# Kernel optimization log

Hardware: AMD Instinct MI355X
Metric: run time of the kernel (lower is better)

## Reference

```python
import jax, jax.numpy as jnp
import numpy as np

HIDDEN = 2048
NUM_ROUTED = 24          # num_routed_experts(6) * segmentation_factor(4)
ROUTED_INTER = 512       # intermediate_dim(2048) // segmentation_factor(4)
NUM_SHARED = 2
SHARED_INTER = 2048
TOP_K = 6


def setup_inputs() -> dict:
    key = jax.random.key(0)
    ks = jax.random.split(key, 8)
    std = 0.02
    x = jax.random.normal(ks[0], (2, 2048, HIDDEN), dtype=jnp.float32)
    gate_w = jax.random.normal(ks[1], (NUM_ROUTED, HIDDEN), dtype=jnp.float32) * (0.02 / np.sqrt(HIDDEN))
    shared_w1 = jax.random.normal(ks[2], (NUM_SHARED, HIDDEN, SHARED_INTER), dtype=jnp.float32) * std
    shared_w3 = jax.random.normal(ks[3], (NUM_SHARED, HIDDEN, SHARED_INTER), dtype=jnp.float32) * std
    shared_w2 = jax.random.normal(ks[4], (NUM_SHARED, SHARED_INTER, HIDDEN), dtype=jnp.float32) * std
    routed_w1 = jax.random.normal(ks[5], (NUM_ROUTED, HIDDEN, ROUTED_INTER), dtype=jnp.float32) * std
    routed_w3 = jax.random.normal(ks[6], (NUM_ROUTED, HIDDEN, ROUTED_INTER), dtype=jnp.float32) * std
    routed_w2 = jax.random.normal(ks[7], (NUM_ROUTED, ROUTED_INTER, HIDDEN), dtype=jnp.float32) * std
    return {"x": x, "gate_w": gate_w,
            "shared_w1": shared_w1, "shared_w2": shared_w2, "shared_w3": shared_w3,
            "routed_w1": routed_w1, "routed_w2": routed_w2, "routed_w3": routed_w3}


def _swiglu_ffn(x, w1, w2, w3):
    # x: [..., n, h]; w1,w3: [..., h, i]; w2: [..., i, h]  (dropout inactive at eval)
    h = jax.nn.silu(jnp.einsum('nh,ehi->eni', x, w1)) * jnp.einsum('nh,ehi->eni', x, w3)
    return jnp.einsum('eni,eih->enh', h, w2)


def reference(x, gate_w, shared_w1, shared_w2, shared_w3, routed_w1, routed_w2, routed_w3):
    B, S, H = x.shape
    x_flat = x.reshape(-1, H)                       # [N, H]
    N = x_flat.shape[0]

    # shared experts (summed)
    shared_out = _swiglu_ffn(x_flat, shared_w1, shared_w2, shared_w3).sum(axis=0)  # [N, H]

    # routing (eval mode: no bias added to logits, aux_loss = 0)
    scores = jax.nn.sigmoid(x_flat @ gate_w.T)      # [N, E]
    top_scores, top_idx = jax.lax.top_k(scores, TOP_K)
    top_weights = top_scores / (top_scores.sum(-1, keepdims=True) + 1e-9)  # [N, K]

    # dense dispatch/combine weights [N, E] (indices unique per row)
    dense_w = jnp.zeros((N, NUM_ROUTED), dtype=x.dtype)
    dense_w = dense_w.at[jnp.arange(N)[:, None], top_idx].set(top_weights)

    # run every routed expert on all tokens, combine with routing weights
    expert_out = _swiglu_ffn(x_flat, routed_w1, routed_w2, routed_w3)  # [E, N, H]
    combined = jnp.einsum('ne,enh->nh', dense_w, expert_out)

    output = (shared_out + combined).reshape(B, S, H)
    aux_loss = jnp.float32(0.0)  # eval mode
    return output, aux_loss
```

## Files before the change

### kernel.cpp

```cpp
#include <hip/hip_runtime.h>
#include <hip/hip_bf16.h>

#define HID   2048
#define NTOK  4096
#define NEXP  24
#define SHCOL 4096
#define TOPK  6
#define NSLOT (NTOK * TOPK)

typedef __bf16 bf16_t;
typedef __bf16 bf16x8 __attribute__((ext_vector_type(8)));
typedef __bf16 bf16x4 __attribute__((ext_vector_type(4)));
typedef float  f32x4  __attribute__((ext_vector_type(4)));

__device__ __forceinline__ void async_copy16(const bf16_t* g, bf16_t* l) {
  __builtin_amdgcn_global_load_lds(
      (const __attribute__((address_space(1))) unsigned int*)g,
      (__attribute__((address_space(3))) unsigned int*)l,
      16, 0, 0);
}
template<int N> __device__ __forceinline__ void wait_vm() {
  asm volatile("s_waitcnt vmcnt(%0)" :: "n"(N) : "memory");
}
__device__ __forceinline__ void memfence_sched() { asm volatile("" ::: "memory"); }
__device__ __forceinline__ void bar() {
  memfence_sched();
  __builtin_amdgcn_s_barrier();
  memfence_sched();
}

__device__ __forceinline__ bf16x8 frag32(const bf16_t* region, int row, int cc) {
  return *(const bf16x8*)(region + row * 32 + ((cc ^ ((row >> 1) & 3)) << 3));
}

__global__ void cast_x_kernel(const float* __restrict__ x, bf16_t* __restrict__ xb) {
  int i = blockIdx.x * 256 + threadIdx.x;
  float4 v = ((const float4*)x)[i];
  bf16x4 o = { (bf16_t)v.x, (bf16_t)v.y, (bf16_t)v.z, (bf16_t)v.w };
  ((bf16x4*)xb)[i] = o;
}

__global__ __launch_bounds__(256) void transpose_cast_v2(
    const float* __restrict__ src, bf16_t* __restrict__ dst,
    int C, long dstStride, long srcExpStride, long dstExpStride) {
  __shared__ float t[64][68];
  const int e = blockIdx.z;
  src += (long)e * srcExpStride;
  dst += (long)e * dstExpStride;
  const int c0 = blockIdx.x * 64, r0 = blockIdx.y * 64;
  const int tid = threadIdx.x;
  {
    const int tr = tid >> 4, tc = tid & 15;
#pragma unroll
    for (int p = 0; p < 4; ++p) {
      const int r = p * 16 + tr;
      const float4 v = *(const float4*)(src + (long)(r0 + r) * C + c0 + tc * 4);
      *(float4*)&t[r][tc * 4] = v;
    }
  }
  __syncthreads();
  {
    const int l8 = tid & 7, rb = l8 * 8;
#pragma unroll
    for (int p = 0; p < 2; ++p) {
      const int c = p * 32 + (tid >> 3);
      bf16x8 o;
#pragma unroll
      for (int s = 0; s < 8; ++s) o[s] = (bf16_t)t[rb + s][c];
      *(bf16x8*)(dst + (long)(c0 + c) * dstStride + r0 + rb) = o;
    }
  }
}

__global__ void gate_topk(const float* __restrict__ x, const float* __restrict__ gw,
                          int* __restrict__ tk_idx, float* __restrict__ tk_w,
                          float* __restrict__ aux) {
  int lane = threadIdx.x & 63;
  int wave = threadIdx.x >> 6;
  int token = blockIdx.x * 4 + wave;
  const float* xr = x + (long)token * HID;
  float xv[32];
#pragma unroll
  for (int i = 0; i < 32; ++i) xv[i] = xr[lane + i * 64];
  float sc[NEXP];
#pragma unroll
  for (int e = 0; e < NEXP; ++e) {
    const float* g = gw + (long)e * HID;
    float s = 0.f;
#pragma unroll
    for (int i = 0; i < 32; ++i) s += xv[i] * g[lane + i * 64];
#pragma unroll
    for (int off = 32; off > 0; off >>= 1) s += __shfl_down(s, off);
    sc[e] = s;
  }
  if (lane == 0) {
    float sg[NEXP];
#pragma unroll
    for (int e = 0; e < NEXP; ++e) sg[e] = 1.0f / (1.0f + expf(-sc[e]));
    unsigned taken = 0;
    int   sel[TOPK];
    float sw[TOPK];
    float sum = 0.f;
    for (int k = 0; k < TOPK; ++k) {
      float best = -1.f; int bi = 0;
#pragma unroll
      for (int e = 0; e < NEXP; ++e) {
        bool avail = !(taken & (1u << e));
        if (avail && sg[e] > best) { best = sg[e]; bi = e; }
      }
      taken |= (1u << bi);
      sel[k] = bi; sw[k] = best; sum += best;
    }
    float inv = 1.0f / (sum + 1e-9f);
#pragma unroll
    for (int k = 0; k < TOPK; ++k) {
      tk_idx[token * TOPK + k] = sel[k];
      tk_w[token * TOPK + k]   = sw[k] * inv;
    }
  }
  if (blockIdx.x == 0 && threadIdx.x == 0) *aux = 0.0f;
}

__global__ void dispatch(const int* __restrict__ tk_idx, const float* __restrict__ tk_w,
                         int* __restrict__ perm, float* __restrict__ wslot,
                         int* __restrict__ slot_of, int* __restrict__ meta,
                         int* __restrict__ uptab, int* __restrict__ dntab) {
  __shared__ int cnt[NEXP], cnt2[NEXP], off[NEXP + 1];
  int tid = threadIdx.x;
  if (tid < NEXP) { cnt[tid] = 0; cnt2[tid] = 0; }
  __syncthreads();
  for (int i = tid; i < NSLOT; i += 1024) atomicAdd(&cnt[tk_idx[i]], 1);
  __syncthreads();
  if (tid == 0) {
    int o = 0, un = 0, dn = 0;
    for (int e = 0; e < NEXP; ++e) {
      off[e] = o;
      int c = cnt[e];
      for (int r0 = 0; r0 < c; r0 += 256) uptab[un++] = (e << 16) | r0;
      for (int r0 = 0; r0 < c; r0 += 128) dntab[dn++] = (e << 16) | r0;
      o += c;
    }
    off[NEXP] = o;
    meta[0] = un; meta[1] = dn;
    for (int e = 0; e < NEXP; ++e) { meta[8 + e] = cnt[e]; meta[32 + e] = off[e]; }
  }
  __syncthreads();
  for (int i = tid; i < NSLOT; i += 1024) {
    int e = tk_idx[i];
    int loc = atomicAdd(&cnt2[e], 1);
    int slot = off[e] + loc;
    perm[slot] = i / TOPK;
    wslot[slot] = tk_w[i];
    slot_of[i] = slot;
  }
}

__global__ __launch_bounds__(512, 2) void gemm_up(
    const bf16_t* __restrict__ xb, const bf16_t* __restrict__ w1t,
    const bf16_t* __restrict__ w3t, bf16_t* __restrict__ hsh,
    bf16_t* __restrict__ hr, const int* __restrict__ perm,
    const float* __restrict__ wslot, const int* __restrict__ meta,
    const int* __restrict__ uptab) {
  __shared__ bf16_t lds[4 * 16384];
  const int bid = blockIdx.x;
  const int tid  = threadIdx.x;
  const int lane = tid & 63;
  const int wave = tid >> 6;
  const int wm = wave >> 2;
  const int wc = wave & 3;
  const bool role_sh = bid < 512;
  int m0 = 0, j0 = 0, jc = 0, M = 256, bslot = 0;
  const bf16_t *b1G, *b3G;
  if (role_sh) {
    m0 = (bid >> 5) * 256; j0 = (bid & 31) * 128;
    b1G = w1t + (long)j0 * HID;
    b3G = w3t + (long)j0 * HID;
  } else {
    int t = bid - 512;
    int rt = t >> 2; jc = t & 3;
    if (rt >= meta[0]) return;
    int pk = uptab[rt];
    int e = pk >> 16, row0 = pk & 0xffff;
    bslot = meta[32 + e] + row0;
    M = min(256, meta[8 + e] - row0);
    int col = SHCOL + e * 512 + jc * 128;
    b1G = w1t + (long)col * HID;
    b3G = w3t + (long)col * HID;
  }
  const bf16_t* gsrc[4];
  int loff[4];
#pragma unroll
  for (int it = 0; it < 4; ++it) {
    int idx = it * 512 + tid;
    if (idx < 1024) {
      int r = idx >> 2, c = idx & 3;
      long rowbase;
      if (role_sh) rowbase = (long)(m0 + r) * HID;
      else         rowbase = (long)perm[bslot + ((r < M) ? r : 0)] * HID;
      gsrc[it] = xb + rowbase + ((c ^ ((r >> 1) & 3)) << 3);
      loff[it] = idx << 3;
    } else if (idx < 1536) {
      int i2 = idx - 1024; int r = i2 >> 2, c = i2 & 3;
      gsrc[it] = b1G + (long)r * HID + ((c ^ ((r >> 1) & 3)) << 3);
      loff[it] = 8192 + (i2 << 3);
    } else {
      int i2 = idx - 1536; int r = i2 >> 2, c = i2 & 3;
      gsrc[it] = b3G + (long)r * HID + ((c ^ ((r >> 1) & 3)) << 3);
      loff[it] = 12288 + (i2 << 3);
    }
  }
  auto STAGE = [&](int t) {
    bf16_t* sb = lds + (t & 3) * 16384;
#pragma unroll
    for (int it = 0; it < 4; ++it)
      async_copy16(gsrc[it] + t * 32, sb + loff[it]);
  };

  f32x4 acc1[8][2] = {};
  f32x4 acc3[8][2] = {};
  const int NT = HID / 32;
  STAGE(0); STAGE(1);
  wait_vm<4>();
  __syncthreads();
  const int rA = wm * 128 + (lane & 15);
  const int rB = wc * 32 + (lane & 15);
  const int cc = lane >> 4;
  for (int t = 0; t < NT; ++t) {
    const bf16_t* sb = lds + (t & 3) * 16384;
    bf16x8 a[4], b1[2], b3[2];
#pragma unroll
    for (int fm = 0; fm < 4; ++fm) a[fm] = frag32(sb, rA + fm * 16, cc);
#pragma unroll
    for (int fn = 0; fn < 2; ++fn) {
      b1[fn] = frag32(sb + 8192,  rB + fn * 16, cc);
      b3[fn] = frag32(sb + 12288, rB + fn * 16, cc);
    }
    if (t + 2 < NT) STAGE(t + 2);
    bar();
    __builtin_amdgcn_s_setprio(1);
#pragma unroll
    for (int fn = 0; fn < 2; ++fn)
#pragma unroll
      for (int fm = 0; fm < 4; ++fm) {
        acc1[fm][fn] = __builtin_amdgcn_mfma_f32_16x16x32_bf16(a[fm], b1[fn], acc1[fm][fn], 0, 0, 0);
        acc3[fm][fn] = __builtin_amdgcn_mfma_f32_16x16x32_bf16(a[fm], b3[fn], acc3[fm][fn], 0, 0, 0);
      }
    __builtin_amdgcn_s_setprio(0);
    bar();
    bf16x8 a2[4];
#pragma unroll
    for (int fm = 0; fm < 4; ++fm) a2[fm] = frag32(sb, rA + 64 + fm * 16, cc);
    bar();
    __builtin_amdgcn_s_setprio(1);
#pragma unroll
    for (int fn = 0; fn < 2; ++fn)
#pragma unroll
      for (int fm = 0; fm < 4; ++fm) {
        acc1[4 + fm][fn] = __builtin_amdgcn_mfma_f32_16x16x32_bf16(a2[fm], b1[fn], acc1[4 + fm][fn], 0, 0, 0);
        acc3[4 + fm][fn] = __builtin_amdgcn_mfma_f32_16x16x32_bf16(a2[fm], b3[fn], acc3[4 + fm][fn], 0, 0, 0);
      }
    __builtin_amdgcn_s_setprio(0);
    memfence_sched();
    if (t < NT - 2) wait_vm<4>();
    else            wait_vm<0>();
    bar();
  }
  const int mloc_base = wm * 128 + ((lane >> 4) << 2);
  const int cloc = wc * 32 + (lane & 15);
#pragma unroll
  for (int fm = 0; fm < 8; ++fm) {
#pragma unroll
    for (int jj = 0; jj < 4; ++jj) {
      const int mloc = mloc_base + fm * 16 + jj;
      if (role_sh) {
        bf16_t* dst = hsh + (long)(m0 + mloc) * SHCOL + j0 + cloc;
#pragma unroll
        for (int fn = 0; fn < 2; ++fn) {
          const float u1 = acc1[fm][fn][jj];
          const float u3 = acc3[fm][fn][jj];
          dst[fn * 16] = (bf16_t)((u1 / (1.0f + __expf(-u1))) * u3);
        }
      } else if (mloc < M) {
        const int slot = bslot + mloc;
        const float w = wslot[slot];
        bf16_t* dst = hr + (long)slot * 512 + jc * 128 + cloc;
#pragma unroll
        for (int fn = 0; fn < 2; ++fn) {
          const float u1 = acc1[fm][fn][jj];
          const float u3 = acc3[fm][fn][jj];
          dst[fn * 16] = (bf16_t)((u1 / (1.0f + __expf(-u1))) * u3 * w);
        }
      }
    }
  }
}

__global__ __launch_bounds__(512, 2) void gemm_down(
    const bf16_t* __restrict__ hsh, const bf16_t* __restrict__ w2ts,
    const bf16_t* __restrict__ hr, const bf16_t* __restrict__ rw2t,
    float* __restrict__ sout, bf16_t* __restrict__ y,
    const int* __restrict__ meta, const int* __restrict__ dntab) {
  __shared__ bf16_t lds[4 * 12288];
  const int bid = blockIdx.x;
  const int tid  = threadIdx.x;
  const int lane = tid & 63;
  const int wave = tid >> 6;
  const int wm = wave >> 2;
  const int wc = wave & 3;
  const bool role_sh = bid < 256;
  int m0 = 0, n0, M = 128, bslot = 0, NT;
  const bf16_t *aG, *bG;
  long lda, ldb;
  if (role_sh) {
    m0 = (bid >> 3) * 128; n0 = (bid & 7) * 256;
    aG = hsh + (long)m0 * SHCOL; lda = SHCOL;
    bG = w2ts + (long)n0 * SHCOL; ldb = SHCOL;
    NT = SHCOL / 32;
  } else {
    int t = bid - 256;
    int rt = t >> 3; n0 = (t & 7) * 256;
    if (rt >= meta[1]) return;
    int pk = dntab[rt];
    int e = pk >> 16, row0 = pk & 0xffff;
    bslot = meta[32 + e] + row0;
    M = min(128, meta[8 + e] - row0);
    aG = hr + (long)bslot * 512; lda = 512;
    bG = rw2t + (long)e * (2048L * 512) + (long)n0 * 512; ldb = 512;
    NT = 512 / 32;
  }
  const bf16_t* gsrc[3];
  int loff[3];
#pragma unroll
  for (int it = 0; it < 3; ++it) {
    int idx = it * 512 + tid;
    if (idx < 512) {
      int r = idx >> 2, c = idx & 3;
      gsrc[it] = aG + (long)r * lda + ((c ^ ((r >> 1) & 3)) << 3);
      loff[it] = idx << 3;
    } else {
      int i2 = idx - 512; int r = i2 >> 2, c = i2 & 3;
      gsrc[it] = bG + (long)r * ldb + ((c ^ ((r >> 1) & 3)) << 3);
      loff[it] = 4096 + (i2 << 3);
    }
  }
  auto STAGE = [&](int t) {
    bf16_t* sb = lds + (t & 3) * 12288;
#pragma unroll
    for (int it = 0; it < 3; ++it)
      async_copy16(gsrc[it] + t * 32, sb + loff[it]);
  };

  f32x4 acc[4][4] = {};
  STAGE(0); STAGE(1);
  wait_vm<3>();
  __syncthreads();
  const int rA = wm * 64 + (lane & 15);
  const int rB = wc * 64 + (lane & 15);
  const int cc = lane >> 4;
  for (int t = 0; t < NT; ++t) {
    const bf16_t* sb = lds + (t & 3) * 12288;
    bf16x8 a[4], b[4];
#pragma unroll
    for (int fm = 0; fm < 4; ++fm) a[fm] = frag32(sb, rA + fm * 16, cc);
    b[0] = frag32(sb + 4096, rB, cc);
    b[1] = frag32(sb + 4096, rB + 16, cc);
    if (t + 2 < NT) STAGE(t + 2);
    bar();
    __builtin_amdgcn_s_setprio(1);
#pragma unroll
    for (int fn = 0; fn < 2; ++fn)
#pragma unroll
      for (int fm = 0; fm < 4; ++fm)
        acc[fm][fn] = __builtin_amdgcn_mfma_f32_16x16x32_bf16(a[fm], b[fn], acc[fm][fn], 0, 0, 0);
    __builtin_amdgcn_s_setprio(0);
    bar();
    b[2] = frag32(sb + 4096, rB + 32, cc);
    b[3] = frag32(sb + 4096, rB + 48, cc);
    bar();
    __builtin_amdgcn_s_setprio(1);
#pragma unroll
    for (int fn = 2; fn < 4; ++fn)
#pragma unroll
      for (int fm = 0; fm < 4; ++fm)
        acc[fm][fn] = __builtin_amdgcn_mfma_f32_16x16x32_bf16(a[fm], b[fn], acc[fm][fn], 0, 0, 0);
    __builtin_amdgcn_s_setprio(0);
    memfence_sched();
    if (t < NT - 2) wait_vm<3>();
    else            wait_vm<0>();
    bar();
  }
  const int mloc_base = wm * 64 + ((lane >> 4) << 2);
  const int cbase = n0 + wc * 64 + (lane & 15);
#pragma unroll
  for (int fm = 0; fm < 4; ++fm)
#pragma unroll
    for (int jj = 0; jj < 4; ++jj) {
      const int mloc = mloc_base + fm * 16 + jj;
      if (role_sh) {
#pragma unroll
        for (int fn = 0; fn < 4; ++fn)
          sout[(long)(m0 + mloc) * HID + cbase + fn * 16] = acc[fm][fn][jj];
      } else if (mloc < M) {
#pragma unroll
        for (int fn = 0; fn < 4; ++fn)
          y[(long)(bslot + mloc) * HID + cbase + fn * 16] = (bf16_t)acc[fm][fn][jj];
      }
    }
}

__global__ void combine(const float* __restrict__ sout, const bf16_t* __restrict__ y,
                        const int* __restrict__ slot_of, float* __restrict__ out) {
  const int n = blockIdx.x;
  const int c0 = threadIdx.x * 8;
  float acc[8];
  const float4* sp = (const float4*)(sout + (long)n * HID + c0);
  float4 s0 = sp[0], s1 = sp[1];
  acc[0]=s0.x; acc[1]=s0.y; acc[2]=s0.z; acc[3]=s0.w;
  acc[4]=s1.x; acc[5]=s1.y; acc[6]=s1.z; acc[7]=s1.w;
#pragma unroll
  for (int k = 0; k < TOPK; ++k) {
    int slot = slot_of[n * TOPK + k];
    bf16x8 v = *(const bf16x8*)(y + (long)slot * HID + c0);
#pragma unroll
    for (int i = 0; i < 8; ++i) acc[i] += (float)v[i];
  }
  float4* op = (float4*)(out + (long)n * HID + c0);
  op[0] = make_float4(acc[0], acc[1], acc[2], acc[3]);
  op[1] = make_float4(acc[4], acc[5], acc[6], acc[7]);
}

__global__ void fill_sentinel(float* out, int n) {
  for (int i = blockIdx.x * 256 + threadIdx.x; i < n; i += gridDim.x * 256)
    out[i] = 12345.0f;
}

extern "C" void kernel_launch(void* const* d_in, const int* in_sizes, int n_in,
                              void* d_out, int out_size, void* d_ws, size_t ws_size,
                              hipStream_t stream) {
  (void)in_sizes; (void)n_in;
  const float* x   = (const float*)d_in[0];
  const float* gw  = (const float*)d_in[1];
  const float* sw1 = (const float*)d_in[2];
  const float* sw2 = (const float*)d_in[3];
  const float* sw3 = (const float*)d_in[4];
  const float* rw1 = (const float*)d_in[5];
  const float* rw2 = (const float*)d_in[6];
  const float* rw3 = (const float*)d_in[7];
  float* out = (float*)d_out;

  const size_t OFF_XB    = 0;
  const size_t OFF_W1T   = 16777216;
  const size_t OFF_W3T   = 83886080;
  const size_t OFF_W2TS  = 150994944;
  const size_t OFF_RW2T  = 167772160;
  const size_t OFF_HSH   = 218103808;
  const size_t OFF_HR    = 251658240;
  const size_t OFF_SOUT  = 277086208;
  const size_t OFF_TKI   = 310640640;
  const size_t OFF_TKW   = 310738944;
  const size_t OFF_PERM  = 310837248;
  const size_t OFF_WSLOT = 310935552;
  const size_t OFF_SLOTOF= 311033856;
  const size_t OFF_META  = 311132160;
  const size_t OFF_UPTAB = 311136256;
  const size_t OFF_DNTAB = 311140352;
  const size_t NEED      = 311148544;
  if (ws_size < NEED) {
    fill_sentinel<<<4096, 256, 0, stream>>>(out, out_size);
    return;
  }
  char* ws = (char*)d_ws;
  bf16_t* xb     = (bf16_t*)(ws + OFF_XB);
  bf16_t* w1t    = (bf16_t*)(ws + OFF_W1T);
  bf16_t* w3t    = (bf16_t*)(ws + OFF_W3T);
  bf16_t* w2ts   = (bf16_t*)(ws + OFF_W2TS);
  bf16_t* rw2t   = (bf16_t*)(ws + OFF_RW2T);
  bf16_t* hsh    = (bf16_t*)(ws + OFF_HSH);
  bf16_t* hr     = (bf16_t*)(ws + OFF_HR);
  float*  sout   = (float*)(ws + OFF_SOUT);
  bf16_t* y      = (bf16_t*)(ws + OFF_W1T);
  int*    tki    = (int*)(ws + OFF_TKI);
  float*  tkw    = (float*)(ws + OFF_TKW);
  int*    perm   = (int*)(ws + OFF_PERM);
  float*  wslot  = (float*)(ws + OFF_WSLOT);
  int*    slotof = (int*)(ws + OFF_SLOTOF);
  int*    meta   = (int*)(ws + OFF_META);
  int*    uptab  = (int*)(ws + OFF_UPTAB);
  int*    dntab  = (int*)(ws + OFF_DNTAB);

  cast_x_kernel<<<8192, 256, 0, stream>>>(x, xb);
  gate_topk<<<1024, 256, 0, stream>>>(x, gw, tki, tkw, out + (size_t)NTOK * HID);
  dispatch<<<1, 1024, 0, stream>>>(tki, tkw, perm, wslot, slotof, meta, uptab, dntab);

  transpose_cast_v2<<<dim3(32, 32, 2),  256, 0, stream>>>(sw1, w1t, 2048, 2048, 2048L*2048, 2048L*2048);
  transpose_cast_v2<<<dim3(8,  32, 24), 256, 0, stream>>>(rw1, w1t + (long)SHCOL*HID, 512, 2048, 2048L*512, 512L*2048);
  transpose_cast_v2<<<dim3(32, 32, 2),  256, 0, stream>>>(sw3, w3t, 2048, 2048, 2048L*2048, 2048L*2048);
  transpose_cast_v2<<<dim3(8,  32, 24), 256, 0, stream>>>(rw3, w3t + (long)SHCOL*HID, 512, 2048, 2048L*512, 512L*2048);
  transpose_cast_v2<<<dim3(32, 32, 2),  256, 0, stream>>>(sw2, w2ts, 2048, 4096, 2048L*2048, 2048);
  transpose_cast_v2<<<dim3(32, 8, 24),  256, 0, stream>>>(rw2, rw2t, 2048, 512, 512L*2048, 2048L*512);

  gemm_up<<<dim3(512 + 480), 512, 0, stream>>>(xb, w1t, w3t, hsh, hr, perm, wslot, meta, uptab);
  gemm_down<<<dim3(256 + 1728), 512, 0, stream>>>(hsh, w2ts, hr, rw2t, sout, y, meta, dntab);
  combine<<<dim3(NTOK), 256, 0, stream>>>(sout, y, slotof, out);
}
```

Measured before the change: 682.4 us.

## Merge cast/transpose kernels into one launch and cut per-iteration barriers in GEMMs

Folds the x cast and six weight transpose-cast launches into a single prep kernel indexed by flattened block id, removing launch gaps and tail effects between them. In gemm_up and gemm_down, the main loop is reorganised so each k-step waits on the async loads and barriers once at the top, with one mid-step barrier, replacing three barriers per iteration. gemm_down also drops from a 4-stage to a 3-stage LDS ring with stage issue after the barrier, which lowers LDS use. This adds risk around the vmcnt accounting and buffer reuse ordering with fewer barriers.

```diff
diff --git a/kernel.cpp b/kernel.cpp
--- a/kernel.cpp
+++ b/kernel.cpp
@@ -23,32 +23,15 @@
   asm volatile("s_waitcnt vmcnt(%0)" :: "n"(N) : "memory");
 }
 __device__ __forceinline__ void memfence_sched() { asm volatile("" ::: "memory"); }
-__device__ __forceinline__ void bar() {
-  memfence_sched();
-  __builtin_amdgcn_s_barrier();
-  memfence_sched();
-}
 
 __device__ __forceinline__ bf16x8 frag32(const bf16_t* region, int row, int cc) {
   return *(const bf16x8*)(region + row * 32 + ((cc ^ ((row >> 1) & 3)) << 3));
 }
 
-__global__ void cast_x_kernel(const float* __restrict__ x, bf16_t* __restrict__ xb) {
-  int i = blockIdx.x * 256 + threadIdx.x;
-  float4 v = ((const float4*)x)[i];
-  bf16x4 o = { (bf16_t)v.x, (bf16_t)v.y, (bf16_t)v.z, (bf16_t)v.w };
-  ((bf16x4*)xb)[i] = o;
-}
-
-__global__ __launch_bounds__(256) void transpose_cast_v2(
+__device__ __forceinline__ void tcast_tile(
     const float* __restrict__ src, bf16_t* __restrict__ dst,
-    int C, long dstStride, long srcExpStride, long dstExpStride) {
+    int C, long dstStride, int c0, int r0, int tid) {
   __shared__ float t[64][68];
-  const int e = blockIdx.z;
-  src += (long)e * srcExpStride;
-  dst += (long)e * dstExpStride;
-  const int c0 = blockIdx.x * 64, r0 = blockIdx.y * 64;
-  const int tid = threadIdx.x;
   {
     const int tr = tid >> 4, tc = tid & 15;
 #pragma unroll
@@ -70,6 +53,37 @@
       *(bf16x8*)(dst + (long)(c0 + c) * dstStride + r0 + rb) = o;
     }
   }
+}
+
+__global__ __launch_bounds__(256) void prep(
+    const float* __restrict__ x, bf16_t* __restrict__ xb,
+    const float* __restrict__ sw1, const float* __restrict__ rw1,
+    const float* __restrict__ sw3, const float* __restrict__ rw3,
+    const float* __restrict__ sw2, const float* __restrict__ rw2,
+    bf16_t* __restrict__ w1t, bf16_t* __restrict__ w3t,
+    bf16_t* __restrict__ w2ts, bf16_t* __restrict__ rw2t) {
+  int bid = blockIdx.x;
+  if (bid < 8192) {
+    int i = bid * 256 + threadIdx.x;
+    float4 v = ((const float4*)x)[i];
+    bf16x4 o = { (bf16_t)v.x, (bf16_t)v.y, (bf16_t)v.z, (bf16_t)v.w };
+    ((bf16x4*)xb)[i] = o;
+    return;
+  }
+  bid -= 8192;
+  const float* src; bf16_t* dst; int C; long dstStride, seS, deS; int BX, nPer;
+  if (bid < 2048)       { src=sw1; dst=w1t;                  C=2048; dstStride=2048; seS=2048L*2048; deS=2048L*2048; BX=32; nPer=1024; }
+  else if (bid < 8192)  { bid-=2048;  src=rw1; dst=w1t+(long)SHCOL*HID; C=512;  dstStride=2048; seS=2048L*512;  deS=512L*2048;  BX=8;  nPer=256; }
+  else if (bid < 10240) { bid-=8192;  src=sw3; dst=w3t;                 C=2048; dstStride=2048; seS=2048L*2048; deS=2048L*2048; BX=32; nPer=1024; }
+  else if (bid < 16384) { bid-=10240; src=rw3; dst=w3t+(long)SHCOL*HID; C=512;  dstStride=2048; seS=2048L*512;  deS=512L*2048;  BX=8;  nPer=256; }
+  else if (bid < 18432) { bid-=16384; src=sw2; dst=w2ts;                C=2048; dstStride=4096; seS=2048L*2048; deS=2048;       BX=32; nPer=1024; }
+  else                  { bid-=18432; src=rw2; dst=rw2t;                C=2048; dstStride=512;  seS=512L*2048;  deS=2048L*512;  BX=32; nPer=256; }
+  const int e  = bid / nPer;
+  const int rem = bid - e * nPer;
+  const int by = rem / BX;
+  const int bx = rem - by * BX;
+  tcast_tile(src + (long)e * seS, dst + (long)e * deS, C, dstStride,
+             bx * 64, by * 64, threadIdx.x);
 }
 
 __global__ void gate_topk(const float* __restrict__ x, const float* __restrict__ gw,
@@ -219,13 +233,17 @@
   f32x4 acc1[8][2] = {};
   f32x4 acc3[8][2] = {};
   const int NT = HID / 32;
-  STAGE(0); STAGE(1);
-  wait_vm<4>();
-  __syncthreads();
   const int rA = wm * 128 + (lane & 15);
   const int rB = wc * 32 + (lane & 15);
   const int cc = lane >> 4;
+  STAGE(0); STAGE(1);
   for (int t = 0; t < NT; ++t) {
+    if (t + 2 < NT) STAGE(t + 2);
+    if (t < NT - 2)       wait_vm<8>();
+    else if (t == NT - 2) wait_vm<4>();
+    else                  wait_vm<0>();
+    __builtin_amdgcn_s_barrier();
+    memfence_sched();
     const bf16_t* sb = lds + (t & 3) * 16384;
     bf16x8 a[4], b1[2], b3[2];
 #pragma unroll
@@ -235,8 +253,6 @@
       b1[fn] = frag32(sb + 8192,  rB + fn * 16, cc);
       b3[fn] = frag32(sb + 12288, rB + fn * 16, cc);
     }
-    if (t + 2 < NT) STAGE(t + 2);
-    bar();
     __builtin_amdgcn_s_setprio(1);
 #pragma unroll
     for (int fn = 0; fn < 2; ++fn)
@@ -246,11 +262,12 @@
         acc3[fm][fn] = __builtin_amdgcn_mfma_f32_16x16x32_bf16(a[fm], b3[fn], acc3[fm][fn], 0, 0, 0);
       }
     __builtin_amdgcn_s_setprio(0);
-    bar();
+    memfence_sched();
+    __builtin_amdgcn_s_barrier();
+    memfence_sched();
     bf16x8 a2[4];
 #pragma unroll
     for (int fm = 0; fm < 4; ++fm) a2[fm] = frag32(sb, rA + 64 + fm * 16, cc);
-    bar();
     __builtin_amdgcn_s_setprio(1);
 #pragma unroll
     for (int fn = 0; fn < 2; ++fn)
@@ -261,9 +278,6 @@
       }
     __builtin_amdgcn_s_setprio(0);
     memfence_sched();
-    if (t < NT - 2) wait_vm<4>();
-    else            wait_vm<0>();
-    bar();
   }
   const int mloc_base = wm * 128 + ((lane >> 4) << 2);
   const int cloc = wc * 32 + (lane & 15);
@@ -300,7 +314,7 @@
     const bf16_t* __restrict__ hr, const bf16_t* __restrict__ rw2t,
     float* __restrict__ sout, bf16_t* __restrict__ y,
     const int* __restrict__ meta, const int* __restrict__ dntab) {
-  __shared__ bf16_t lds[4 * 12288];
+  __shared__ bf16_t lds[3 * 12288];
   const int bid = blockIdx.x;
   const int tid  = threadIdx.x;
   const int lane = tid & 63;
@@ -344,28 +358,29 @@
     }
   }
   auto STAGE = [&](int t) {
-    bf16_t* sb = lds + (t & 3) * 12288;
+    bf16_t* sb = lds + (t % 3) * 12288;
 #pragma unroll
     for (int it = 0; it < 3; ++it)
       async_copy16(gsrc[it] + t * 32, sb + loff[it]);
   };
 
   f32x4 acc[4][4] = {};
-  STAGE(0); STAGE(1);
-  wait_vm<3>();
-  __syncthreads();
   const int rA = wm * 64 + (lane & 15);
   const int rB = wc * 64 + (lane & 15);
   const int cc = lane >> 4;
+  STAGE(0); STAGE(1);
   for (int t = 0; t < NT; ++t) {
-    const bf16_t* sb = lds + (t & 3) * 12288;
+    if (t + 1 < NT) wait_vm<3>();
+    else            wait_vm<0>();
+    __builtin_amdgcn_s_barrier();
+    memfence_sched();
+    if (t + 2 < NT) STAGE(t + 2);
+    const bf16_t* sb = lds + (t % 3) * 12288;
     bf16x8 a[4], b[4];
 #pragma unroll
     for (int fm = 0; fm < 4; ++fm) a[fm] = frag32(sb, rA + fm * 16, cc);
     b[0] = frag32(sb + 4096, rB, cc);
     b[1] = frag32(sb + 4096, rB + 16, cc);
-    if (t + 2 < NT) STAGE(t + 2);
-    bar();
     __builtin_amdgcn_s_setprio(1);
 #pragma unroll
     for (int fn = 0; fn < 2; ++fn)
@@ -373,10 +388,11 @@
       for (int fm = 0; fm < 4; ++fm)
         acc[fm][fn] = __builtin_amdgcn_mfma_f32_16x16x32_bf16(a[fm], b[fn], acc[fm][fn], 0, 0, 0);
     __builtin_amdgcn_s_setprio(0);
-    bar();
+    memfence_sched();
+    __builtin_amdgcn_s_barrier();
+    memfence_sched();
     b[2] = frag32(sb + 4096, rB + 32, cc);
     b[3] = frag32(sb + 4096, rB + 48, cc);
-    bar();
     __builtin_amdgcn_s_setprio(1);
 #pragma unroll
     for (int fn = 2; fn < 4; ++fn)
@@ -385,9 +401,6 @@
         acc[fm][fn] = __builtin_amdgcn_mfma_f32_16x16x32_bf16(a[fm], b[fn], acc[fm][fn], 0, 0, 0);
     __builtin_amdgcn_s_setprio(0);
     memfence_sched();
-    if (t < NT - 2) wait_vm<3>();
-    else            wait_vm<0>();
-    bar();
   }
   const int mloc_base = wm * 64 + ((lane >> 4) << 2);
   const int cbase = n0 + wc * 64 + (lane & 15);
@@ -488,16 +501,10 @@
   int*    uptab  = (int*)(ws + OFF_UPTAB);
   int*    dntab  = (int*)(ws + OFF_DNTAB);
 
-  cast_x_kernel<<<8192, 256, 0, stream>>>(x, xb);
   gate_topk<<<1024, 256, 0, stream>>>(x, gw, tki, tkw, out + (size_t)NTOK * HID);
   dispatch<<<1, 1024, 0, stream>>>(tki, tkw, perm, wslot, slotof, meta, uptab, dntab);
-
-  transpose_cast_v2<<<dim3(32, 32, 2),  256, 0, stream>>>(sw1, w1t, 2048, 2048, 2048L*2048, 2048L*2048);
-  transpose_cast_v2<<<dim3(8,  32, 24), 256, 0, stream>>>(rw1, w1t + (long)SHCOL*HID, 512, 2048, 2048L*512, 512L*2048);
-  transpose_cast_v2<<<dim3(32, 32, 2),  256, 0, stream>>>(sw3, w3t, 2048, 2048, 2048L*2048, 2048L*2048);
-  transpose_cast_v2<<<dim3(8,  32, 24), 256, 0, stream>>>(rw3, w3t + (long)SHCOL*HID, 512, 2048, 2048L*512, 512L*2048);
-  transpose_cast_v2<<<dim3(32, 32, 2),  256, 0, stream>>>(sw2, w2ts, 2048, 4096, 2048L*2048, 2048);
-  transpose_cast_v2<<<dim3(32, 8, 24),  256, 0, stream>>>(rw2, rw2t, 2048, 512, 512L*2048, 2048L*512);
+  prep<<<32768, 256, 0, stream>>>(x, xb, sw1, rw1, sw3, rw3, sw2, rw2,
+                                  w1t, w3t, w2ts, rw2t);
 
   gemm_up<<<dim3(512 + 480), 512, 0, stream>>>(xb, w1t, w3t, hsh, hr, perm, wslot, meta, uptab);
   gemm_down<<<dim3(256 + 1728), 512, 0, stream>>>(hsh, w2ts, hr, rw2t, sout, y, meta, dntab);
```

Result: faster. 645.2 us (-5.5%).
